# Kernel tuning notes

Hardware: AMD Instinct MI355X
Metric: run time of the kernel (lower is better)

## Reference

```python
import jax, jax.numpy as jnp
import numpy as np

B, N, T, M, DIM = 4, 4096, 16, 64, 1024
HEADS, DH = 8, 64
INNER = HEADS * DH  # 512
KV = T * M          # 1024


def setup_inputs() -> dict:
    key = jax.random.key(0)
    ks = jax.random.split(key, 8)
    x = jax.random.normal(ks[0], (B, N, DIM), jnp.float32)
    media = jax.random.normal(ks[1], (B, T, M, DIM), jnp.float32)
    # sparse media markers so cumsum(text_time) stays within [0, T]
    media_locations = jax.random.uniform(ks[2], (B, N)) < (T / N)
    ln_scale = jnp.ones((DIM,), jnp.float32)
    ln_bias = jnp.zeros((DIM,), jnp.float32)
    s_in = DIM ** -0.5
    Wq = jax.random.normal(ks[3], (DIM, INNER), jnp.float32) * s_in
    Wk = jax.random.normal(ks[4], (DIM, INNER), jnp.float32) * s_in
    Wv = jax.random.normal(ks[5], (DIM, INNER), jnp.float32) * s_in
    Wo = jax.random.normal(ks[6], (INNER, DIM), jnp.float32) * (INNER ** -0.5)
    return dict(x=x, media=media, media_locations=media_locations,
                ln_scale=ln_scale, ln_bias=ln_bias, Wq=Wq, Wk=Wk, Wv=Wv, Wo=Wo)


def reference(x, media, media_locations, ln_scale, ln_bias, Wq, Wk, Wv, Wo):
    scale = DH ** -0.5
    # LayerNorm(eps=1e-5)
    mu = jnp.mean(x, axis=-1, keepdims=True)
    var = jnp.mean((x - mu) ** 2, axis=-1, keepdims=True)
    xn = (x - mu) / jnp.sqrt(var + 1e-5) * ln_scale + ln_bias

    q = xn @ Wq                                   # [b, n, inner]
    media_f = media.reshape(B, KV, DIM)           # b (t m) d
    k = media_f @ Wk                              # [b, kv, inner]
    v = media_f @ Wv

    q = q.reshape(B, N, HEADS, DH).transpose(0, 2, 1, 3) * scale  # b h n d
    k = k.reshape(B, KV, HEADS, DH).transpose(0, 2, 1, 3)         # b h kv d
    v = v.reshape(B, KV, HEADS, DH).transpose(0, 2, 1, 3)

    sim = jnp.einsum('bhid,bhjd->bhij', q, k)     # [b, h, n, kv]

    # media-location mask: each text token attends only to its immediately
    # preceding media item (only_attend_immediate_media=True -> eq)
    text_time = jnp.cumsum(media_locations.astype(jnp.int32), axis=-1)  # [b, n]
    media_time = jnp.repeat(jnp.arange(1, T + 1), M)                    # [kv]
    mask = text_time[:, None, :, None] == media_time[None, None, None, :]
    sim = jnp.where(mask, sim, -jnp.finfo(sim.dtype).max)

    attn = jax.nn.softmax(sim, axis=-1)  # stable (subtracts rowmax), same math
    # NOTE: the original's masked_fill_ of attn for media-less text tokens is a
    # no-op (return value discarded), faithfully omitted here.

    out = jnp.einsum('bhij,bhjd->bhid', attn, v)  # b h n d
    out = out.transpose(0, 2, 1, 3).reshape(B, N, INNER)
    return out @ Wo
```

## Files before the change

### kernel.cpp

```cpp
#include <hip/hip_runtime.h>

using u16 = unsigned short;
using uch = unsigned char;

typedef __bf16 bf16x8 __attribute__((ext_vector_type(8)));
typedef float f32x4 __attribute__((ext_vector_type(4)));

#define BATCH 4
#define SEQN 4096
#define TT 16
#define MM 64
#define DIM 1024
#define HEADS 8
#define DH 64
#define INNER 512
#define KVN 1024
#define NTOK (BATCH*SEQN)
#define MAXBLK 352

#define FB_WT0  1
#define FB_CVT0 2049
#define FB_LN0  6145
#define FB_GRID (FB_LN0 + NTOK)

#define OFF_XN     ((size_t)0)
#define OFF_MEDIA  ((size_t)33554432)
#define OFF_Q      ((size_t)41943040)
#define OFF_KV     ((size_t)58720256)
#define OFF_AOUT   ((size_t)67108864)
#define OFF_WQT    ((size_t)83886080)
#define OFF_WKVT   ((size_t)84934656)
#define OFF_WOT    ((size_t)87031808)
#define OFF_VSUM   ((size_t)88145920)
#define OFF_FLAGS  ((size_t)88154112)
#define OFF_VT     ((size_t)88155136)
#define OFF_NBLK   ((size_t)92350464)
#define OFF_DESC   ((size_t)92351488)

__device__ __forceinline__ u16 f2bf(float f){
  unsigned int u = __float_as_uint(f);
  u += 0x7fffu + ((u >> 16) & 1u);
  return (u16)(u >> 16);
}
__device__ __forceinline__ float bf2f(u16 b){ return __uint_as_float(((unsigned int)b) << 16); }

__device__ __forceinline__ void async16(const u16* g, void* l){
  __builtin_amdgcn_global_load_lds((__attribute__((address_space(1))) void*)(g),
                                   (__attribute__((address_space(3))) void*)(l), 16, 0, 0);
}

__device__ __forceinline__ int detect_bf16(const unsigned int* __restrict__ x){
  __shared__ int scnt;
  const int tid = threadIdx.x;
  if (tid == 0) scnt = 0;
  __syncthreads();
  int c = 0;
  #pragma unroll
  for (int t = 0; t < 4; ++t){
    unsigned int w = x[t*256 + tid];
    unsigned int e = (w >> 7) & 0xFFu;
    c += (e >= 110u && e <= 140u) ? 1 : 0;
  }
  #pragma unroll
  for (int o = 32; o > 0; o >>= 1) c += __shfl_down(c, o);
  if ((tid & 63) == 0) atomicAdd(&scnt, c);
  __syncthreads();
  return scnt > 512 ? 1 : 0;
}

__global__ __launch_bounds__(256) void front_kernel(
    const unsigned int* __restrict__ x, const uch* __restrict__ loc,
    const void* __restrict__ ln_g, const void* __restrict__ ln_b,
    const void* __restrict__ media,
    const void* __restrict__ Wq, const void* __restrict__ Wk,
    const void* __restrict__ Wv, const void* __restrict__ Wo,
    u16* __restrict__ xn, u16* __restrict__ medb,
    u16* __restrict__ WqT, u16* __restrict__ WkvT, u16* __restrict__ WoT,
    int* __restrict__ flags, float* __restrict__ vsum,
    int4* __restrict__ desc, int* __restrict__ nblk){
  const int bid = blockIdx.x, tid = threadIdx.x;

  if (bid == 0){
    __shared__ int nonzS;
    __shared__ int wsumS[4];
    __shared__ int sbound[4][19];
    __shared__ int gcnt[72];
    int bf = detect_bf16(x);
    if (tid == 0) nonzS = 0;
    if (tid < 76) sbound[tid/19][tid%19] = 4096;
    #pragma unroll
    for (int t = 0; t < 8; ++t) vsum[t*256 + tid] = 0.f;
    __syncthreads();
    int nz = 0;
    #pragma unroll
    for (int t = 0; t < 16; ++t){
      int i = t*256 + tid;
      if ((i & 3) && loc[i]) nz++;
    }
    #pragma unroll
    for (int o = 32; o > 0; o >>= 1) nz += __shfl_down(nz, o);
    if ((tid & 63) == 0) atomicAdd(&nonzS, nz);
    __syncthreads();
    const int as32 = (nonzS == 0) ? 1 : 0;
    if (tid == 0){ flags[0] = bf; flags[1] = as32; }
    const int lane = tid & 63, wl = tid >> 6;
    for (int b = 0; b < BATCH; ++b){
      int v[16];
      if (as32){
        const int4* p = (const int4*)((const int*)loc + b*SEQN + tid*16);
        #pragma unroll
        for (int j = 0; j < 4; ++j){
          int4 q = p[j];
          v[j*4+0]=q.x!=0; v[j*4+1]=q.y!=0; v[j*4+2]=q.z!=0; v[j*4+3]=q.w!=0;
        }
      } else {
        const uchar4* p = (const uchar4*)(loc + b*SEQN + tid*16);
        #pragma unroll
        for (int j = 0; j < 4; ++j){
          uchar4 q = p[j];
          v[j*4+0]=q.x!=0; v[j*4+1]=q.y!=0; v[j*4+2]=q.z!=0; v[j*4+3]=q.w!=0;
        }
      }
      int tsum = 0;
      #pragma unroll
      for (int j = 0; j < 16; ++j) tsum += v[j];
      int s = tsum;
      #pragma unroll
      for (int o = 1; o < 64; o <<= 1){ int n2 = __shfl_up(s, o); if (lane >= o) s += n2; }
      if (lane == 63) wsumS[wl] = s;
      __syncthreads();
      int base = 0;
      for (int w2 = 0; w2 < wl; ++w2) base += wsumS[w2];
      int tt = base + s - tsum;
      #pragma unroll
      for (int j = 0; j < 16; ++j){
        if (v[j]){ tt++; if (tt <= 17) sbound[b][tt] = tid*16 + j; }
      }
      __syncthreads();
    }
    if (tid < 72){
      int bb = tid/18, g = tid%18;
      int lo = (g == 0) ? 0 : sbound[bb][g];
      int hi = (g < 17) ? sbound[bb][g+1] : 4096;
      if (hi < lo) hi = lo;
      gcnt[tid] = (hi - lo + 63) >> 6;
    }
    __syncthreads();
    if (tid == 0){
      int acc = 0;
      for (int i = 0; i < 72; ++i){ int c2 = gcnt[i]; gcnt[i] = acc; acc += c2; }
      *nblk = acc;
    }
    __syncthreads();
    if (tid < 72){
      int bb = tid/18, g = tid%18;
      int lo = (g == 0) ? 0 : sbound[bb][g];
      int hi = (g < 17) ? sbound[bb][g+1] : 4096;
      if (hi < lo) hi = lo;
      int s2 = (g == 0 || g == 17) ? -1 : (g - 1);
      int n0 = gcnt[tid];
      for (int k = lo, j = 0; k < hi; k += 64, ++j){
        int4 d; d.x = bb; d.y = s2; d.z = bb*4096 + k; d.w = min(64, hi - k);
        desc[n0 + j] = d;
      }
    }
    return;
  }

  if (bid < FB_CVT0){
    const int bf = detect_bf16(x);
    __shared__ float tile[32][33];
    int id = bid - FB_WT0;
    const void* in; u16* out; int K, N, bx, by;
    if (id < 512){       in = Wq; out = WqT;  K = DIM;   N = INNER; bx = id & 15; by = id >> 4; }
    else if (id < 1024){ in = Wk; out = WkvT; K = DIM;   N = INNER; int l = id - 512;  bx = l & 15; by = l >> 4; }
    else if (id < 1536){ in = Wv; out = WkvT + (size_t)512*1024; K = DIM; N = INNER; int l = id - 1024; bx = l & 15; by = l >> 4; }
    else {               in = Wo; out = WoT;  K = INNER; N = DIM;   int l = id - 1536; bx = l & 31; by = l >> 5; }
    int n0 = bx*32, k0 = by*32;
    int tx = tid & 31, ty = tid >> 5;
    #pragma unroll
    for (int i = 0; i < 4; ++i){
      size_t idx = (size_t)(k0 + ty + i*8)*N + n0 + tx;
      tile[ty + i*8][tx] = bf ? bf2f(((const u16*)in)[idx]) : ((const float*)in)[idx];
    }
    __syncthreads();
    #pragma unroll
    for (int i = 0; i < 4; ++i)
      out[(size_t)(n0 + ty + i*8)*K + k0 + tx] = f2bf(tile[tx][ty + i*8]);
    return;
  }

  if (bid < FB_LN0){
    const int bf = detect_bf16(x);
    size_t i = (size_t)(bid - FB_CVT0)*256 + tid;
    if (bf){
      ((ushort4*)medb)[i] = ((const ushort4*)media)[i];
    } else {
      float4 t = ((const float4*)media)[i];
      ushort4 o; o.x = f2bf(t.x); o.y = f2bf(t.y); o.z = f2bf(t.z); o.w = f2bf(t.w);
      ((ushort4*)medb)[i] = o;
    }
    return;
  }

  const int bf = detect_bf16(x);
  const int row = bid - FB_LN0;
  float v[4];
  if (bf){
    ushort4 t = ((const ushort4*)((const u16*)x + (size_t)row*DIM))[tid];
    v[0]=bf2f(t.x); v[1]=bf2f(t.y); v[2]=bf2f(t.z); v[3]=bf2f(t.w);
  } else {
    float4 t = ((const float4*)((const float*)x + (size_t)row*DIM))[tid];
    v[0]=t.x; v[1]=t.y; v[2]=t.z; v[3]=t.w;
  }
  float s = v[0]+v[1]+v[2]+v[3];
  float sq = v[0]*v[0]+v[1]*v[1]+v[2]*v[2]+v[3]*v[3];
  #pragma unroll
  for (int o = 32; o > 0; o >>= 1){ s += __shfl_down(s, o); sq += __shfl_down(sq, o); }
  __shared__ float ss[4], ssq[4];
  int wid = tid >> 6, lane = tid & 63;
  if (lane == 0){ ss[wid] = s; ssq[wid] = sq; }
  __syncthreads();
  s = ss[0]+ss[1]+ss[2]+ss[3]; sq = ssq[0]+ssq[1]+ssq[2]+ssq[3];
  float mean = s * (1.f/DIM);
  float rstd = rsqrtf(sq * (1.f/DIM) - mean*mean + 1e-5f);
  float g[4], bb[4];
  if (bf){
    ushort4 t1 = ((const ushort4*)ln_g)[tid]; ushort4 t2 = ((const ushort4*)ln_b)[tid];
    g[0]=bf2f(t1.x); g[1]=bf2f(t1.y); g[2]=bf2f(t1.z); g[3]=bf2f(t1.w);
    bb[0]=bf2f(t2.x); bb[1]=bf2f(t2.y); bb[2]=bf2f(t2.z); bb[3]=bf2f(t2.w);
  } else {
    float4 t1 = ((const float4*)ln_g)[tid]; float4 t2 = ((const float4*)ln_b)[tid];
    g[0]=t1.x; g[1]=t1.y; g[2]=t1.z; g[3]=t1.w;
    bb[0]=t2.x; bb[1]=t2.y; bb[2]=t2.z; bb[3]=t2.w;
  }
  ushort4 o;
  o.x = f2bf((v[0]-mean)*rstd*g[0] + bb[0]);
  o.y = f2bf((v[1]-mean)*rstd*g[1] + bb[1]);
  o.z = f2bf((v[2]-mean)*rstd*g[2] + bb[2]);
  o.w = f2bf((v[3]-mean)*rstd*g[3] + bb[3]);
  ((ushort4*)(xn + (size_t)row*DIM))[tid] = o;
}

template<int ROWS>
__device__ __forceinline__ void g8_stage(const u16* __restrict__ src, char* dst, int K, int t,
                                         int tid, int wid){
  #pragma unroll
  for (int i = 0; i < ROWS/64; ++i){
    int s_ = i*512 + tid;
    int row_ = s_ >> 3, g_ = s_ & 7;
    async16(src + (size_t)row_*K + t*64 + ((g_ ^ (row_ & 7)) << 3),
            dst + (size_t)(i*512 + wid*64)*16);
  }
}

template<int BN, int NT, int MODE>
__device__ __forceinline__ void gemm8_body(const u16* __restrict__ A, const u16* __restrict__ Bt,
                        void* __restrict__ Cp, int Nglob, float alpha, const int* __restrict__ flags,
                        int rm, int rn, u16* sA0, u16* sA1, u16* sB0, u16* sB1,
                        u16* __restrict__ vtp, float* __restrict__ vsum){
  constexpr int K = NT*64;
  constexpr int NREP = BN/64;
  const int tid = threadIdx.x, wid = tid >> 6, lane = tid & 63;
  const int wr = wid >> 2, wc = wid & 3;
  const int lr = lane & 15, lg = lane >> 4;
  f32x4 acc[8][NREP] = {};
  const u16* Ab = A + (size_t)rm*256*K;
  const u16* Bb = Bt + (size_t)rn*BN*K;

  g8_stage<256>(Ab, (char*)sA0, K, 0, tid, wid);
  g8_stage<BN >(Bb, (char*)sB0, K, 0, tid, wid);
  __syncthreads();

  for (int t = 0; t < NT; ++t){
    u16* Acur = (t & 1) ? sA1 : sA0;
    u16* Bcur = (t & 1) ? sB1 : sB0;
    u16* Anxt = (t & 1) ? sA0 : sA1;
    u16* Bnxt = (t & 1) ? sB0 : sB1;
    bf16x8 bfr[NREP][2];
    #pragma unroll
    for (int p = 0; p < 4; ++p){
      if (p == 0 && t + 1 < NT){
        g8_stage<256>(Ab, (char*)Anxt, K, t+1, tid, wid);
        g8_stage<BN >(Bb, (char*)Bnxt, K, t+1, tid, wid);
      }
      bf16x8 af[2][2];
      #pragma unroll
      for (int i = 0; i < 2; ++i){
        int row = wr*128 + (2*p + i)*16 + lr;
        #pragma unroll
        for (int ks = 0; ks < 2; ++ks){
          int g = (ks*4 + lg) ^ (row & 7);
          af[i][ks] = *(const bf16x8*)((const char*)Acur + row*128 + g*16);
        }
      }
      if (p == 0){
        #pragma unroll
        for (int n = 0; n < NREP; ++n){
          int row = wc*(BN/4) + n*16 + lr;
          #pragma unroll
          for (int ks = 0; ks < 2; ++ks){
            int g = (ks*4 + lg) ^ (row & 7);
            bfr[n][ks] = *(const bf16x8*)((const char*)Bcur + row*128 + g*16);
          }
        }
      }
      __builtin_amdgcn_s_barrier();
      __builtin_amdgcn_s_setprio(1);
      #pragma unroll
      for (int i = 0; i < 2; ++i)
        #pragma unroll
        for (int n = 0; n < NREP; ++n)
          #pragma unroll
          for (int ks = 0; ks < 2; ++ks)
            acc[2*p + i][n] = __builtin_amdgcn_mfma_f32_16x16x32_bf16(af[i][ks], bfr[n][ks], acc[2*p + i][n], 0, 0, 0);
      __builtin_amdgcn_s_setprio(0);
      __builtin_amdgcn_s_barrier();
    }
    if (t + 1 < NT) __syncthreads();
  }

  if (MODE == 2){
    #pragma unroll
    for (int n = 0; n < NREP; ++n){
      int col = rn*BN + wc*(BN/4) + n*16 + lr;
      float psum = 0.f;
      #pragma unroll
      for (int m = 0; m < 8; ++m){
        int row0 = rm*256 + wr*128 + m*16 + lg*4;
        #pragma unroll
        for (int r = 0; r < 4; ++r){
          float v = acc[m][n][r];
          psum += v;
          int row = row0 + r;
          u16 bv = f2bf(v);
          ((u16*)Cp)[(size_t)row*Nglob + col] = bv;
          if (col >= 512){
            int kvi = row & 1023;
            int s = kvi >> 6, rr = kvi & 63;
            vtp[((size_t)(((row >> 10)*16 + s)*512 + (col - 512)))*64 + rr] = bv;
          }
        }
      }
      if (col >= 512) atomicAdd(&vsum[(rm >> 2)*512 + (col - 512)], psum);
    }
    return;
  }

  const bool obf = (MODE == 0) || (flags[0] != 0);
  #pragma unroll
  for (int m = 0; m < 8; ++m){
    #pragma unroll
    for (int n = 0; n < NREP; ++n){
      int row0 = rm*256 + wr*128 + m*16 + lg*4;
      int col  = rn*BN + wc*(BN/4) + n*16 + lr;
      #pragma unroll
      for (int r = 0; r < 4; ++r){
        float v = acc[m][n][r] * alpha;
        size_t idx = (size_t)(row0 + r)*Nglob + col;
        if (obf) ((u16*)Cp)[idx] = f2bf(v);
        else     ((float*)Cp)[idx] = v;
      }
    }
  }
}

__global__ __launch_bounds__(512) void proj_kernel(
    const u16* __restrict__ xn, const u16* __restrict__ WqT, u16* __restrict__ qb,
    const u16* __restrict__ medb, const u16* __restrict__ WkvT, u16* __restrict__ kvb,
    u16* __restrict__ vtp, float* __restrict__ vsum, const int* __restrict__ flags){
  __shared__ u16 smem[49152];
  u16* sA0 = smem;          u16* sA1 = smem + 16384;
  u16* sB0 = smem + 32768;  u16* sB1 = smem + 40960;
  if (blockIdx.x < 256){
    int bid = blockIdx.x;
    int wg = (bid & 7)*32 + (bid >> 3);
    gemm8_body<128, 16, 0>(xn, WqT, qb, INNER, 0.125f, flags, wg >> 2, wg & 3,
                           sA0, sA1, sB0, sB1, nullptr, nullptr);
  } else {
    int bid = blockIdx.x - 256;
    int wg = (bid & 7)*16 + (bid >> 3);
    gemm8_body<128, 16, 2>(medb, WkvT, kvb, 1024, 1.f, flags, wg >> 3, wg & 7,
                           sA0, sA1, sB0, sB1, vtp, vsum);
  }
}

__global__ __launch_bounds__(512) void gemm8_out_kernel(const u16* __restrict__ A,
                        const u16* __restrict__ Bt, void* __restrict__ Cp,
                        const int* __restrict__ flags){
  __shared__ u16 As[2][16384];
  __shared__ u16 Bs[2][16384];
  int flat = blockIdx.x + blockIdx.y*gridDim.x;
  int wg = (flat & 7)*32 + (flat >> 3);
  int rn = wg & 3, rm = wg >> 2;
  gemm8_body<256, 8, 1>(A, Bt, Cp, DIM, 1.f, flags, rm, rn, As[0], As[1], Bs[0], Bs[1],
                        nullptr, nullptr);
}

__global__ __launch_bounds__(256) void attn2_kernel(
    const u16* __restrict__ qb, const u16* __restrict__ kvb, const u16* __restrict__ vt,
    const int* __restrict__ nblk, const int4* __restrict__ desc,
    const float* __restrict__ vsum, u16* __restrict__ aout){
  __shared__ u16 Ks[64*64];
  __shared__ u16 Vs[64*64];
  __shared__ u16 Ps[4][16*72];
  if (blockIdx.x >= *nblk) return;
  const int4 d = desc[blockIdx.x];
  const int b = d.x, s = d.y, rowStart = d.z, cnt = d.w;
  const int h = blockIdx.y;
  const int tid = threadIdx.x, w = tid >> 6, lane = tid & 63;
  if (s < 0){
    const float inv = 1.f/1024.f;
    for (int idx = tid; idx < cnt*64; idx += 256){
      int slot = idx >> 6, c = h*64 + (idx & 63);
      aout[(size_t)(rowStart + slot)*512 + c] = f2bf(vsum[b*512 + c]*inv);
    }
    return;
  }
  const int lr = lane & 15, lg = lane >> 4;
  const size_t kbase = ((size_t)(b*1024 + s*64))*1024;
  const size_t vbase = ((size_t)(b*16 + s))*512*64;
  const int myslot = w*16 + lr;
  const size_t qrow = (size_t)(rowStart + min(myslot, cnt - 1))*512;
  #pragma unroll
  for (int t = 0; t < 2; ++t){
    int ci = t*256 + tid;
    int r = ci >> 3, q = ci & 7;
    int qs = (q ^ (r & 7)) << 3;
    async16(kvb + kbase + (size_t)r*1024 + h*64 + qs, (char*)Ks + ci*16);
    async16(vt + vbase + (size_t)(h*64 + r)*64 + qs, (char*)Vs + ci*16);
  }
  __syncthreads();
  bf16x8 qa0 = *(const bf16x8*)(qb + qrow + h*64 + lg*8);
  bf16x8 qa1 = *(const bf16x8*)(qb + qrow + h*64 + 32 + lg*8);
  f32x4 sv[4] = {};
  #pragma unroll
  for (int n = 0; n < 4; ++n){
    int row = n*16 + lr;
    int sl0 = (lg) ^ (row & 7);
    int sl1 = (4 + lg) ^ (row & 7);
    bf16x8 kb0 = *(const bf16x8*)((const char*)Ks + row*128 + sl0*16);
    sv[n] = __builtin_amdgcn_mfma_f32_16x16x32_bf16(qa0, kb0, sv[n], 0, 0, 0);
    bf16x8 kb1 = *(const bf16x8*)((const char*)Ks + row*128 + sl1*16);
    sv[n] = __builtin_amdgcn_mfma_f32_16x16x32_bf16(qa1, kb1, sv[n], 0, 0, 0);
  }
  float inv[4];
  #pragma unroll
  for (int r = 0; r < 4; ++r){
    float m = fmaxf(fmaxf(sv[0][r], sv[1][r]), fmaxf(sv[2][r], sv[3][r]));
    #pragma unroll
    for (int o = 1; o < 16; o <<= 1) m = fmaxf(m, __shfl_xor(m, o));
    float s0 = 0.f;
    #pragma unroll
    for (int n = 0; n < 4; ++n){ sv[n][r] = __expf(sv[n][r] - m); s0 += sv[n][r]; }
    #pragma unroll
    for (int o = 1; o < 16; o <<= 1) s0 += __shfl_xor(s0, o);
    inv[r] = 1.f / s0;
  }
  u16* pw = &Ps[w][0];
  #pragma unroll
  for (int n = 0; n < 4; ++n)
    #pragma unroll
    for (int r = 0; r < 4; ++r)
      pw[(4*lg + r)*72 + n*16 + lr] = f2bf(sv[n][r] * inv[r]);
  bf16x8 pa0 = *(const bf16x8*)((const char*)pw + lr*144 + lg*16);
  bf16x8 pa1 = *(const bf16x8*)((const char*)pw + lr*144 + 64 + lg*16);
  f32x4 ov[4] = {};
  #pragma unroll
  for (int n = 0; n < 4; ++n){
    int row = n*16 + lr;
    int sl0 = (lg) ^ (row & 7);
    int sl1 = (4 + lg) ^ (row & 7);
    bf16x8 vb0 = *(const bf16x8*)((const char*)Vs + row*128 + sl0*16);
    ov[n] = __builtin_amdgcn_mfma_f32_16x16x32_bf16(pa0, vb0, ov[n], 0, 0, 0);
    bf16x8 vb1 = *(const bf16x8*)((const char*)Vs + row*128 + sl1*16);
    ov[n] = __builtin_amdgcn_mfma_f32_16x16x32_bf16(pa1, vb1, ov[n], 0, 0, 0);
  }
  #pragma unroll
  for (int r = 0; r < 4; ++r){
    int slot = w*16 + 4*lg + r;
    if (slot < cnt){
      size_t orow = (size_t)(rowStart + slot)*512 + h*64;
      #pragma unroll
      for (int n = 0; n < 4; ++n)
        aout[orow + n*16 + lr] = f2bf(ov[n][r]);
    }
  }
}

extern "C" void kernel_launch(void* const* d_in, const int* in_sizes, int n_in,
                              void* d_out, int out_size, void* d_ws, size_t ws_size,
                              hipStream_t stream){
  const void* x      = d_in[0];
  const void* media  = d_in[1];
  const void* mloc   = d_in[2];
  const void* ln_g   = d_in[3];
  const void* ln_b   = d_in[4];
  const void* Wq     = d_in[5];
  const void* Wk     = d_in[6];
  const void* Wv     = d_in[7];
  const void* Wo     = d_in[8];
  char* ws = (char*)d_ws;
  u16* xn    = (u16*)(ws + OFF_XN);
  u16* medb  = (u16*)(ws + OFF_MEDIA);
  u16* qb    = (u16*)(ws + OFF_Q);
  u16* kvb   = (u16*)(ws + OFF_KV);
  u16* aout  = (u16*)(ws + OFF_AOUT);
  u16* WqT   = (u16*)(ws + OFF_WQT);
  u16* WkvT  = (u16*)(ws + OFF_WKVT);
  u16* WoT   = (u16*)(ws + OFF_WOT);
  float* vsm = (float*)(ws + OFF_VSUM);
  int* flags = (int*)(ws + OFF_FLAGS);
  u16* vt    = (u16*)(ws + OFF_VT);
  int* nblk  = (int*)(ws + OFF_NBLK);
  int4* desc = (int4*)(ws + OFF_DESC);

  front_kernel<<<FB_GRID, 256, 0, stream>>>(
      (const unsigned int*)x, (const uch*)mloc, ln_g, ln_b, media,
      Wq, Wk, Wv, Wo, xn, medb, WqT, WkvT, WoT, flags, vsm, desc, nblk);

  proj_kernel<<<384, 512, 0, stream>>>(xn, WqT, qb, medb, WkvT, kvb, vt, vsm, flags);

  attn2_kernel<<<dim3(MAXBLK, 8), 256, 0, stream>>>(qb, kvb, vt, nblk, desc, vsm, aout);

  gemm8_out_kernel<<<dim3(4, 64), 512, 0, stream>>>(aout, WoT, d_out, flags);
}
```

Measured before the change: 131.4 us.

## Use 256x256 tiles in projection GEMM and restructure async prefetch waits

The projection GEMM moves from 256x128 to 256x256 output tiles, halving the block count (384 to 192) and increasing B-operand reuse per block. The double-buffered main loop now issues the next tile's async loads at the top of each iteration, then waits with an explicit s_waitcnt vmcnt(8) and a barrier instead of a trailing __syncthreads. This lets the current tile's loads finish while the next ones stay in flight. The tradeoffs are fewer blocks on a large CU count (192 on MI355X), more accumulator registers and LDS per block, and a vmcnt value hand-tuned to the number of async ops per stage.

```diff
diff --git a/kernel.cpp b/kernel.cpp
--- a/kernel.cpp
+++ b/kernel.cpp
@@ -242,11 +242,10 @@
   ((ushort4*)(xn + (size_t)row*DIM))[tid] = o;
 }
 
-template<int ROWS>
-__device__ __forceinline__ void g8_stage(const u16* __restrict__ src, char* dst, int K, int t,
-                                         int tid, int wid){
-  #pragma unroll
-  for (int i = 0; i < ROWS/64; ++i){
+__device__ __forceinline__ void g8_stage256(const u16* __restrict__ src, char* dst, int K, int t,
+                                            int tid, int wid){
+  #pragma unroll
+  for (int i = 0; i < 4; ++i){
     int s_ = i*512 + tid;
     int row_ = s_ >> 3, g_ = s_ & 7;
     async16(src + (size_t)row_*K + t*64 + ((g_ ^ (row_ & 7)) << 3),
@@ -254,36 +253,39 @@
   }
 }
 
-template<int BN, int NT, int MODE>
+template<int NT, int MODE>
 __device__ __forceinline__ void gemm8_body(const u16* __restrict__ A, const u16* __restrict__ Bt,
                         void* __restrict__ Cp, int Nglob, float alpha, const int* __restrict__ flags,
                         int rm, int rn, u16* sA0, u16* sA1, u16* sB0, u16* sB1,
                         u16* __restrict__ vtp, float* __restrict__ vsum){
   constexpr int K = NT*64;
-  constexpr int NREP = BN/64;
   const int tid = threadIdx.x, wid = tid >> 6, lane = tid & 63;
   const int wr = wid >> 2, wc = wid & 3;
   const int lr = lane & 15, lg = lane >> 4;
-  f32x4 acc[8][NREP] = {};
+  f32x4 acc[8][4] = {};
   const u16* Ab = A + (size_t)rm*256*K;
-  const u16* Bb = Bt + (size_t)rn*BN*K;
-
-  g8_stage<256>(Ab, (char*)sA0, K, 0, tid, wid);
-  g8_stage<BN >(Bb, (char*)sB0, K, 0, tid, wid);
-  __syncthreads();
+  const u16* Bb = Bt + (size_t)rn*256*K;
+
+  g8_stage256(Ab, (char*)sA0, K, 0, tid, wid);
+  g8_stage256(Bb, (char*)sB0, K, 0, tid, wid);
 
   for (int t = 0; t < NT; ++t){
     u16* Acur = (t & 1) ? sA1 : sA0;
     u16* Bcur = (t & 1) ? sB1 : sB0;
     u16* Anxt = (t & 1) ? sA0 : sA1;
     u16* Bnxt = (t & 1) ? sB0 : sB1;
-    bf16x8 bfr[NREP][2];
+    if (t + 1 < NT){
+      g8_stage256(Ab, (char*)Anxt, K, t+1, tid, wid);
+      g8_stage256(Bb, (char*)Bnxt, K, t+1, tid, wid);
+      asm volatile("s_waitcnt vmcnt(8)" ::: "memory");
+    } else {
+      asm volatile("s_waitcnt vmcnt(0)" ::: "memory");
+    }
+    __builtin_amdgcn_s_barrier();
+    __builtin_amdgcn_sched_barrier(0);
+    bf16x8 bfr[4][2];
     #pragma unroll
     for (int p = 0; p < 4; ++p){
-      if (p == 0 && t + 1 < NT){
-        g8_stage<256>(Ab, (char*)Anxt, K, t+1, tid, wid);
-        g8_stage<BN >(Bb, (char*)Bnxt, K, t+1, tid, wid);
-      }
       bf16x8 af[2][2];
       #pragma unroll
       for (int i = 0; i < 2; ++i){
@@ -296,8 +298,8 @@
       }
       if (p == 0){
         #pragma unroll
-        for (int n = 0; n < NREP; ++n){
-          int row = wc*(BN/4) + n*16 + lr;
+        for (int n = 0; n < 4; ++n){
+          int row = wc*64 + n*16 + lr;
           #pragma unroll
           for (int ks = 0; ks < 2; ++ks){
             int g = (ks*4 + lg) ^ (row & 7);
@@ -310,20 +312,20 @@
       #pragma unroll
       for (int i = 0; i < 2; ++i)
         #pragma unroll
-        for (int n = 0; n < NREP; ++n)
+        for (int n = 0; n < 4; ++n)
           #pragma unroll
           for (int ks = 0; ks < 2; ++ks)
             acc[2*p + i][n] = __builtin_amdgcn_mfma_f32_16x16x32_bf16(af[i][ks], bfr[n][ks], acc[2*p + i][n], 0, 0, 0);
       __builtin_amdgcn_s_setprio(0);
       __builtin_amdgcn_s_barrier();
     }
-    if (t + 1 < NT) __syncthreads();
   }
 
   if (MODE == 2){
-    #pragma unroll
-    for (int n = 0; n < NREP; ++n){
-      int col = rn*BN + wc*(BN/4) + n*16 + lr;
+    const int batch = rm >> 2;
+    #pragma unroll
+    for (int n = 0; n < 4; ++n){
+      int col = rn*256 + wc*64 + n*16 + lr;
       float psum = 0.f;
       #pragma unroll
       for (int m = 0; m < 8; ++m){
@@ -342,18 +344,17 @@
           }
         }
       }
-      if (col >= 512) atomicAdd(&vsum[(rm >> 2)*512 + (col - 512)], psum);
+      if (col >= 512) atomicAdd(&vsum[batch*512 + (col - 512)], psum);
     }
     return;
   }
-
   const bool obf = (MODE == 0) || (flags[0] != 0);
   #pragma unroll
   for (int m = 0; m < 8; ++m){
     #pragma unroll
-    for (int n = 0; n < NREP; ++n){
+    for (int n = 0; n < 4; ++n){
       int row0 = rm*256 + wr*128 + m*16 + lg*4;
-      int col  = rn*BN + wc*(BN/4) + n*16 + lr;
+      int col  = rn*256 + wc*64 + n*16 + lr;
       #pragma unroll
       for (int r = 0; r < 4; ++r){
         float v = acc[m][n][r] * alpha;
@@ -369,19 +370,18 @@
     const u16* __restrict__ xn, const u16* __restrict__ WqT, u16* __restrict__ qb,
     const u16* __restrict__ medb, const u16* __restrict__ WkvT, u16* __restrict__ kvb,
     u16* __restrict__ vtp, float* __restrict__ vsum, const int* __restrict__ flags){
-  __shared__ u16 smem[49152];
-  u16* sA0 = smem;          u16* sA1 = smem + 16384;
-  u16* sB0 = smem + 32768;  u16* sB1 = smem + 40960;
-  if (blockIdx.x < 256){
+  __shared__ u16 As[2][16384];
+  __shared__ u16 Bs[2][16384];
+  if (blockIdx.x < 128){
     int bid = blockIdx.x;
-    int wg = (bid & 7)*32 + (bid >> 3);
-    gemm8_body<128, 16, 0>(xn, WqT, qb, INNER, 0.125f, flags, wg >> 2, wg & 3,
-                           sA0, sA1, sB0, sB1, nullptr, nullptr);
+    int wg = (bid & 7)*16 + (bid >> 3);
+    gemm8_body<16, 0>(xn, WqT, qb, INNER, 0.125f, flags, wg >> 1, wg & 1,
+                      As[0], As[1], Bs[0], Bs[1], nullptr, nullptr);
   } else {
-    int bid = blockIdx.x - 256;
-    int wg = (bid & 7)*16 + (bid >> 3);
-    gemm8_body<128, 16, 2>(medb, WkvT, kvb, 1024, 1.f, flags, wg >> 3, wg & 7,
-                           sA0, sA1, sB0, sB1, vtp, vsum);
+    int bid = blockIdx.x - 128;
+    int wg = (bid & 7)*8 + (bid >> 3);
+    gemm8_body<16, 2>(medb, WkvT, kvb, 1024, 1.f, flags, wg >> 2, wg & 3,
+                      As[0], As[1], Bs[0], Bs[1], vtp, vsum);
   }
 }
 
@@ -393,8 +393,8 @@
   int flat = blockIdx.x + blockIdx.y*gridDim.x;
   int wg = (flat & 7)*32 + (flat >> 3);
   int rn = wg & 3, rm = wg >> 2;
-  gemm8_body<256, 8, 1>(A, Bt, Cp, DIM, 1.f, flags, rm, rn, As[0], As[1], Bs[0], Bs[1],
-                        nullptr, nullptr);
+  gemm8_body<8, 1>(A, Bt, Cp, DIM, 1.f, flags, rm, rn, As[0], As[1], Bs[0], Bs[1],
+                   nullptr, nullptr);
 }
 
 __global__ __launch_bounds__(256) void attn2_kernel(
@@ -519,7 +519,7 @@
       (const unsigned int*)x, (const uch*)mloc, ln_g, ln_b, media,
       Wq, Wk, Wv, Wo, xn, medb, WqT, WkvT, WoT, flags, vsm, desc, nblk);
 
-  proj_kernel<<<384, 512, 0, stream>>>(xn, WqT, qb, medb, WkvT, kvb, vt, vsm, flags);
+  proj_kernel<<<192, 512, 0, stream>>>(xn, WqT, qb, medb, WkvT, kvb, vt, vsm, flags);
 
   attn2_kernel<<<dim3(MAXBLK, 8), 256, 0, stream>>>(qb, kvb, vt, nblk, desc, vsm, aout);
 
```

After: 145.2 us. +10.5%, slower.
